# Optimization experiments

Measured on AMD Instinct MI355X. Metric: run time of the kernel, lower is better.

The kernel has to match this reference:

```python
import jax, jax.numpy as jnp
import numpy as np

N = 4096      # particles
E = 262144    # interacting pairs (~64 neighbors each)
H = 128       # MLP hidden width
FD = 6        # force/velocity DOF (force + torque)
FEAT = 7      # rel(3) + dist + r_sq + r_quad + min_dist
IN_DIM = FEAT + 2 * FD  # 19


def setup_inputs() -> dict:
    key = jax.random.key(0)
    ks = jax.random.split(key, 10)
    rel_vecs = jax.random.normal(ks[0], (N, N, 3), jnp.float32)
    target_indices = jax.random.randint(ks[1], (E,), 0, N, dtype=jnp.int64)
    source_indices = jax.random.randint(ks[2], (E,), 0, N, dtype=jnp.int64)
    force = jax.random.normal(ks[3], (N, FD), jnp.float32)
    viscosity = jnp.ones((1,), jnp.float32)
    s1 = 1.0 / np.sqrt(IN_DIM)
    s2 = 1.0 / np.sqrt(H)
    W1 = jax.random.normal(ks[4], (IN_DIM, H), jnp.float32) * s1
    b1 = jnp.zeros((H,), jnp.float32)
    W2 = jax.random.normal(ks[5], (H, H), jnp.float32) * s2
    b2 = jnp.zeros((H,), jnp.float32)
    W3 = jax.random.normal(ks[6], (H, FD), jnp.float32) * s2
    b3 = jnp.zeros((FD,), jnp.float32)
    median = jnp.float32(2.5)
    contact_distance = jnp.float32(2.0)
    return {
        'rel_vecs': rel_vecs, 'target_indices': target_indices,
        'source_indices': source_indices, 'force': force,
        'viscosity': viscosity, 'median': median,
        'contact_distance': contact_distance,
        'W1': W1, 'b1': b1, 'W2': W2, 'b2': b2, 'W3': W3, 'b3': b3,
    }


def _predict_velocity(features, f_t, f_s, mu, W1, b1, W2, b2, W3, b3):
    # MLP over concatenated pair features + both forces; Stokes flow is
    # linear in force/viscosity, so scale output by 1/mu.
    x = jnp.concatenate([features, f_t, f_s], axis=-1)  # [E, 19]
    h = jax.nn.relu(x @ W1 + b1)
    h = jax.nn.relu(h @ W2 + b2)
    return (h @ W3 + b3) / mu  # [E, FD]


def reference(rel_vecs, target_indices, source_indices, force, viscosity,
              median, contact_distance, W1, b1, W2, b2, W3, b3):
    # Gather pairwise relative vectors: [E, 3]
    rel_selected = rel_vecs[target_indices, source_indices]
    dist = jnp.maximum(
        jnp.linalg.norm(rel_selected, axis=-1, keepdims=True), 1e-8)  # [E,1]
    r_shift = dist - median
    r_sq = r_shift * r_shift
    r_quad = r_sq * r_sq
    min_dist = dist - contact_distance
    features = jnp.concatenate(
        [rel_selected, dist, r_sq, r_quad, min_dist], axis=-1)  # [E, 7]
    force_target = force[target_indices]  # [E, FD]
    force_source = force[source_indices]  # [E, FD]
    mu = jnp.asarray(viscosity, dtype=force.dtype).reshape(())
    vel = _predict_velocity(features, force_target, force_source, mu,
                            W1, b1, W2, b2, W3, b3)  # [E, FD]
    # Scatter-add per-target contributions
    contribution = jnp.zeros_like(force).at[target_indices].add(vel)
    return contribution
```

## Files before the change

kernel.cpp:

```cpp
#include <hip/hip_runtime.h>

#define NPART 4096
#define E_TOT 262144
#define HID   128
#define FDOF  6
#define BM    64
#define NIT   (E_TOT / BM)
#define GRID  768
#define XPAD  48
#define HPAD  136

typedef __bf16 bf16x8 __attribute__((ext_vector_type(8)));
typedef float  f32x4  __attribute__((ext_vector_type(4)));

__global__ void pairvel_zero_kernel(float* __restrict__ out, int n) {
    const int i = blockIdx.x * blockDim.x + threadIdx.x;
    if (i < n) out[i] = 0.0f;
}

__global__ __launch_bounds__(256) void pairvel_mfma_kernel(
    const float* __restrict__ rel,
    const int*   __restrict__ tgt,
    const int*   __restrict__ src,
    const float* __restrict__ force,
    const float* __restrict__ visc,
    const float* __restrict__ medianp,
    const float* __restrict__ contactp,
    const float* __restrict__ W1,
    const float* __restrict__ b1,
    const float* __restrict__ W2,
    const float* __restrict__ b2,
    const float* __restrict__ W3,
    const float* __restrict__ b3,
    float* __restrict__ out)
{
    const int tid = threadIdx.x;
    const int w   = tid >> 6;
    const int l   = tid & 63;
    const int l15 = l & 15;
    const int lhi = l >> 4;

    bf16x8 w1f[2], w2f[4][2], w3f[4];
    #pragma unroll
    for (int nb = 0; nb < 2; ++nb) {
        const int n = (2 * w + nb) * 16 + l15;
        #pragma unroll
        for (int r = 0; r < 8; ++r) {
            const int k = lhi * 8 + r;
            w1f[nb][r] = (k < 19) ? (__bf16)W1[k * HID + n] : (__bf16)0.0f;
        }
    }
    #pragma unroll
    for (int kt = 0; kt < 4; ++kt)
        #pragma unroll
        for (int nb = 0; nb < 2; ++nb) {
            const int n = (2 * w + nb) * 16 + l15;
            #pragma unroll
            for (int r = 0; r < 8; ++r)
                w2f[kt][nb][r] = (__bf16)W2[(kt * 32 + lhi * 8 + r) * HID + n];
        }
    #pragma unroll
    for (int kt = 0; kt < 4; ++kt)
        #pragma unroll
        for (int r = 0; r < 8; ++r) {
            const int k = kt * 32 + lhi * 8 + r;
            w3f[kt][r] = (l15 < FDOF) ? (__bf16)W3[k * FDOF + l15] : (__bf16)0.0f;
        }

    const float b1v0 = b1[(2 * w) * 16 + l15];
    const float b1v1 = b1[(2 * w + 1) * 16 + l15];
    const float b2v0 = b2[(2 * w) * 16 + l15];
    const float b2v1 = b2[(2 * w + 1) * 16 + l15];
    const float b3v  = (l15 < FDOF) ? b3[l15] : 0.0f;
    const float inv_mu  = 1.0f / visc[0];
    const float median  = medianp[0];
    const float contact = contactp[0];

    __shared__ __align__(16) __bf16 Xs[2][BM][XPAD];
    __shared__ __align__(16) __bf16 H1s[BM][HPAD];
    __shared__ __align__(16) __bf16 H2s[BM][HPAD];
    __shared__ int tgts[2][BM];

    for (int t = tid; t < 2 * BM * 13; t += 256) {
        const int b = t / (BM * 13), rem = t % (BM * 13);
        Xs[b][rem / 13][19 + rem % 13] = (__bf16)0.0f;
    }

    int   p_i0 = 0;
    float p_v0 = 0.f, p_v1 = 0.f, p_v2 = 0.f;
    float p_f3 = 0.f, p_f4 = 0.f, p_f5 = 0.f;

    auto gather_load = [&](int e0n) {
        if (tid < BM) {
            const int eg = e0n + tid;
            p_i0 = tgt[eg];
            const int sg = src[eg];
            const float* rp = rel + ((size_t)p_i0 * NPART + sg) * 3;
            p_v0 = rp[0]; p_v1 = rp[1]; p_v2 = rp[2];
        } else if (tid < 2 * BM) {
            const int eg = e0n + (tid - BM);
            const float2* f2 =
                reinterpret_cast<const float2*>(force + (size_t)tgt[eg] * FDOF);
            const float2 u0 = f2[0], u1 = f2[1], u2 = f2[2];
            p_v0 = u0.x; p_v1 = u0.y; p_v2 = u1.x;
            p_f3 = u1.y; p_f4 = u2.x; p_f5 = u2.y;
        } else if (tid < 3 * BM) {
            const int eg = e0n + (tid - 2 * BM);
            const float2* f2 =
                reinterpret_cast<const float2*>(force + (size_t)src[eg] * FDOF);
            const float2 u0 = f2[0], u1 = f2[1], u2 = f2[2];
            p_v0 = u0.x; p_v1 = u0.y; p_v2 = u1.x;
            p_f3 = u1.y; p_f4 = u2.x; p_f5 = u2.y;
        }
    };

    auto write_x = [&](int b) {
        if (tid < BM) {
            const int e = tid;
            tgts[b][e] = p_i0;
            const float dist = fmaxf(
                sqrtf(p_v0 * p_v0 + p_v1 * p_v1 + p_v2 * p_v2), 1e-8f);
            const float rs = (dist - median) * (dist - median);
            Xs[b][e][0] = (__bf16)p_v0;
            Xs[b][e][1] = (__bf16)p_v1;
            Xs[b][e][2] = (__bf16)p_v2;
            Xs[b][e][3] = (__bf16)dist;
            Xs[b][e][4] = (__bf16)rs;
            Xs[b][e][5] = (__bf16)(rs * rs);
            Xs[b][e][6] = (__bf16)(dist - contact);
        } else if (tid < 2 * BM) {
            const int e = tid - BM;
            Xs[b][e][7]  = (__bf16)p_v0;
            Xs[b][e][8]  = (__bf16)p_v1;
            Xs[b][e][9]  = (__bf16)p_v2;
            Xs[b][e][10] = (__bf16)p_f3;
            Xs[b][e][11] = (__bf16)p_f4;
            Xs[b][e][12] = (__bf16)p_f5;
        } else if (tid < 3 * BM) {
            const int e = tid - 2 * BM;
            Xs[b][e][13] = (__bf16)p_v0;
            Xs[b][e][14] = (__bf16)p_v1;
            Xs[b][e][15] = (__bf16)p_v2;
            Xs[b][e][16] = (__bf16)p_f3;
            Xs[b][e][17] = (__bf16)p_f4;
            Xs[b][e][18] = (__bf16)p_f5;
        }
    };

    gather_load(blockIdx.x * BM);
    write_x(0);
    int buf = 0;

    for (int it = blockIdx.x; it < NIT; it += GRID) {
        __syncthreads();

        #pragma unroll
        for (int m = 0; m < 4; ++m) {
            const bf16x8 a = *reinterpret_cast<const bf16x8*>(
                &Xs[buf][m * 16 + l15][lhi * 8]);
            #pragma unroll
            for (int nb = 0; nb < 2; ++nb) {
                const float bv = nb ? b1v1 : b1v0;
                f32x4 acc = { bv, bv, bv, bv };
                acc = __builtin_amdgcn_mfma_f32_16x16x32_bf16(
                          a, w1f[nb], acc, 0, 0, 0);
                #pragma unroll
                for (int r = 0; r < 4; ++r)
                    H1s[m * 16 + lhi * 4 + r][(2 * w + nb) * 16 + l15] =
                        (__bf16)fmaxf(acc[r], 0.0f);
            }
        }

        const bool havenext = (it + GRID) < NIT;
        if (havenext) gather_load((it + GRID) * BM);

        __syncthreads();

        #pragma unroll
        for (int m = 0; m < 4; ++m) {
            f32x4 acc0 = { b2v0, b2v0, b2v0, b2v0 };
            f32x4 acc1 = { b2v1, b2v1, b2v1, b2v1 };
            #pragma unroll
            for (int kt = 0; kt < 4; ++kt) {
                const bf16x8 a = *reinterpret_cast<const bf16x8*>(
                    &H1s[m * 16 + l15][kt * 32 + lhi * 8]);
                acc0 = __builtin_amdgcn_mfma_f32_16x16x32_bf16(
                           a, w2f[kt][0], acc0, 0, 0, 0);
                acc1 = __builtin_amdgcn_mfma_f32_16x16x32_bf16(
                           a, w2f[kt][1], acc1, 0, 0, 0);
            }
            #pragma unroll
            for (int r = 0; r < 4; ++r) {
                H2s[m * 16 + lhi * 4 + r][(2 * w) * 16 + l15] =
                    (__bf16)fmaxf(acc0[r], 0.0f);
                H2s[m * 16 + lhi * 4 + r][(2 * w + 1) * 16 + l15] =
                    (__bf16)fmaxf(acc1[r], 0.0f);
            }
        }

        if (havenext) write_x(buf ^ 1);

        __syncthreads();

        f32x4 acc3 = { 0.0f, 0.0f, 0.0f, 0.0f };
        #pragma unroll
        for (int kt = 0; kt < 4; ++kt) {
            const bf16x8 a = *reinterpret_cast<const bf16x8*>(
                &H2s[w * 16 + l15][kt * 32 + lhi * 8]);
            acc3 = __builtin_amdgcn_mfma_f32_16x16x32_bf16(
                       a, w3f[kt], acc3, 0, 0, 0);
        }
        if (l15 < FDOF) {
            #pragma unroll
            for (int r = 0; r < 4; ++r) {
                const int e = w * 16 + lhi * 4 + r;
                atomicAdd(&out[(size_t)tgts[buf][e] * FDOF + l15],
                          (acc3[r] + b3v) * inv_mu);
            }
        }
        buf ^= 1;
    }
}

extern "C" void kernel_launch(void* const* d_in, const int* in_sizes, int n_in,
                              void* d_out, int out_size, void* d_ws, size_t ws_size,
                              hipStream_t stream) {
    const float* rel   = (const float*)d_in[0];
    const int*   tgt   = (const int*)d_in[1];
    const int*   src   = (const int*)d_in[2];
    const float* force = (const float*)d_in[3];
    const float* visc  = (const float*)d_in[4];
    const float* med   = (const float*)d_in[5];
    const float* con   = (const float*)d_in[6];
    const float* W1    = (const float*)d_in[7];
    const float* b1    = (const float*)d_in[8];
    const float* W2    = (const float*)d_in[9];
    const float* b2    = (const float*)d_in[10];
    const float* W3    = (const float*)d_in[11];
    const float* b3    = (const float*)d_in[12];
    float* out = (float*)d_out;

    pairvel_zero_kernel<<<(out_size + 255) / 256, 256, 0, stream>>>(out, out_size);
    pairvel_mfma_kernel<<<GRID, 256, 0, stream>>>(
        rel, tgt, src, force, visc, med, con, W1, b1, W2, b2, W3, b3, out);
}
```

Baseline: 54.49 us.

## Merge hidden LDS buffers, deepen gather prefetch, and raise grid size

Merges the H1 and H2 shared-memory tiles into one buffer, holding the layer-2 accumulators in registers and adding a barrier before overwriting the buffer. This cuts LDS use, which together with the smaller X padding could allow more blocks per CU; the grid grows from 768 to 1024 blocks. The gather prefetch now runs two iterations ahead, giving global loads more time to land. The costs are an extra barrier per iteration, more live registers for the accumulators, and a larger grid that leaves some blocks with one fewer tile.

```diff
diff --git a/kernel.cpp b/kernel.cpp
--- a/kernel.cpp
+++ b/kernel.cpp
@@ -6,8 +6,8 @@
 #define FDOF  6
 #define BM    64
 #define NIT   (E_TOT / BM)
-#define GRID  768
-#define XPAD  48
+#define GRID  1024
+#define XPAD  40
 #define HPAD  136
 
 typedef __bf16 bf16x8 __attribute__((ext_vector_type(8)));
@@ -77,8 +77,7 @@
     const float contact = contactp[0];
 
     __shared__ __align__(16) __bf16 Xs[2][BM][XPAD];
-    __shared__ __align__(16) __bf16 H1s[BM][HPAD];
-    __shared__ __align__(16) __bf16 H2s[BM][HPAD];
+    __shared__ __align__(16) __bf16 Hs[BM][HPAD];
     __shared__ int tgts[2][BM];
 
     for (int t = tid; t < 2 * BM * 13; t += 256) {
@@ -149,6 +148,7 @@
 
     gather_load(blockIdx.x * BM);
     write_x(0);
+    if (blockIdx.x + GRID < NIT) gather_load((blockIdx.x + GRID) * BM);
     int buf = 0;
 
     for (int it = blockIdx.x; it < NIT; it += GRID) {
@@ -166,47 +166,48 @@
                           a, w1f[nb], acc, 0, 0, 0);
                 #pragma unroll
                 for (int r = 0; r < 4; ++r)
-                    H1s[m * 16 + lhi * 4 + r][(2 * w + nb) * 16 + l15] =
+                    Hs[m * 16 + lhi * 4 + r][(2 * w + nb) * 16 + l15] =
                         (__bf16)fmaxf(acc[r], 0.0f);
             }
         }
-
-        const bool havenext = (it + GRID) < NIT;
-        if (havenext) gather_load((it + GRID) * BM);
-
-        __syncthreads();
-
+        __syncthreads();
+
+        f32x4 accs[4][2];
         #pragma unroll
         for (int m = 0; m < 4; ++m) {
-            f32x4 acc0 = { b2v0, b2v0, b2v0, b2v0 };
-            f32x4 acc1 = { b2v1, b2v1, b2v1, b2v1 };
+            accs[m][0] = (f32x4){ b2v0, b2v0, b2v0, b2v0 };
+            accs[m][1] = (f32x4){ b2v1, b2v1, b2v1, b2v1 };
             #pragma unroll
             for (int kt = 0; kt < 4; ++kt) {
                 const bf16x8 a = *reinterpret_cast<const bf16x8*>(
-                    &H1s[m * 16 + l15][kt * 32 + lhi * 8]);
-                acc0 = __builtin_amdgcn_mfma_f32_16x16x32_bf16(
-                           a, w2f[kt][0], acc0, 0, 0, 0);
-                acc1 = __builtin_amdgcn_mfma_f32_16x16x32_bf16(
-                           a, w2f[kt][1], acc1, 0, 0, 0);
+                    &Hs[m * 16 + l15][kt * 32 + lhi * 8]);
+                accs[m][0] = __builtin_amdgcn_mfma_f32_16x16x32_bf16(
+                                 a, w2f[kt][0], accs[m][0], 0, 0, 0);
+                accs[m][1] = __builtin_amdgcn_mfma_f32_16x16x32_bf16(
+                                 a, w2f[kt][1], accs[m][1], 0, 0, 0);
             }
-            #pragma unroll
-            for (int r = 0; r < 4; ++r) {
-                H2s[m * 16 + lhi * 4 + r][(2 * w) * 16 + l15] =
-                    (__bf16)fmaxf(acc0[r], 0.0f);
-                H2s[m * 16 + lhi * 4 + r][(2 * w + 1) * 16 + l15] =
-                    (__bf16)fmaxf(acc1[r], 0.0f);
-            }
-        }
-
-        if (havenext) write_x(buf ^ 1);
-
+        }
+        __syncthreads();
+
+        #pragma unroll
+        for (int m = 0; m < 4; ++m)
+            #pragma unroll
+            for (int nb = 0; nb < 2; ++nb)
+                #pragma unroll
+                for (int r = 0; r < 4; ++r)
+                    Hs[m * 16 + lhi * 4 + r][(2 * w + nb) * 16 + l15] =
+                        (__bf16)fmaxf(accs[m][nb][r], 0.0f);
+
+        if (it + GRID < NIT) write_x(buf ^ 1);
+        if (it + 2 * GRID < NIT)
+            gather_load((it + 2 * GRID) * BM);
         __syncthreads();
 
         f32x4 acc3 = { 0.0f, 0.0f, 0.0f, 0.0f };
         #pragma unroll
         for (int kt = 0; kt < 4; ++kt) {
             const bf16x8 a = *reinterpret_cast<const bf16x8*>(
-                &H2s[w * 16 + l15][kt * 32 + lhi * 8]);
+                &Hs[w * 16 + l15][kt * 32 + lhi * 8]);
             acc3 = __builtin_amdgcn_mfma_f32_16x16x32_bf16(
                        a, w3f[kt], acc3, 0, 0, 0);
         }
```

Result: faster. 49.35 us (-9.4%).
